# Kernel optimization log

Hardware: AMD Instinct MI355X
Metric: run time of the kernel (lower is better)

The kernel has to match this reference:

```python
import jax, jax.numpy as jnp
import numpy as np

N_HEAD = 16


def setup_inputs() -> dict:
    key = jax.random.key(0)
    ks = jax.random.split(key, 12)
    B, T, S, D = 64, 1, 448, 1024
    x = jax.random.normal(ks[0], (B, T, D), dtype=jnp.float32)
    k_cache = jax.random.normal(ks[1], (B, S, D), dtype=jnp.float32)
    v_cache = jax.random.normal(ks[2], (B, S, D), dtype=jnp.float32)
    current_index = jax.random.randint(ks[3], (1,), 0, S, dtype=jnp.int64)
    attention_mask = jnp.zeros((1, S), dtype=jnp.float32)
    s = 0.02
    Wq = jax.random.normal(ks[4], (D, D), dtype=jnp.float32) * s
    bq = jax.random.normal(ks[5], (D,), dtype=jnp.float32) * s
    Wk = jax.random.normal(ks[6], (D, D), dtype=jnp.float32) * s  # whisper key proj has no bias
    Wv = jax.random.normal(ks[7], (D, D), dtype=jnp.float32) * s
    bv = jax.random.normal(ks[8], (D,), dtype=jnp.float32) * s
    Wo = jax.random.normal(ks[9], (D, D), dtype=jnp.float32) * s
    bo = jax.random.normal(ks[10], (D,), dtype=jnp.float32) * s
    return {"x": x, "k_cache": k_cache, "v_cache": v_cache,
            "current_index": current_index, "attention_mask": attention_mask,
            "Wq": Wq, "bq": bq, "Wk": Wk, "Wv": Wv, "bv": bv, "Wo": Wo, "bo": bo}


def reference(x, k_cache, v_cache, current_index, attention_mask,
              Wq, bq, Wk, Wv, bv, Wo, bo):
    B, T, D = x.shape            # T == 1 (single decode token)
    S = k_cache.shape[1]         # cache length (448)
    H = N_HEAD
    Dh = D // H
    scale = float(Dh) ** -0.25

    # q/k/v projections of the new token
    q = x @ Wq + bq              # [B, T, D]
    k = x @ Wk                   # [B, T, D]
    v = x @ Wv + bv              # [B, T, D]

    # scatter the new token into the caches at current_index (functional clone+write)
    idx = current_index[0]
    k_upd = jax.lax.dynamic_update_slice(k_cache, k, (0, idx, 0))  # [B, S, D]
    v_upd = jax.lax.dynamic_update_slice(v_cache, v, (0, idx, 0))

    # whisper qkv_attention: scale q and k each by Dh**-0.25
    qh = q.reshape(B, T, H, Dh).transpose(0, 2, 1, 3) * scale      # [B, H, T, Dh]
    kh = k_upd.reshape(B, S, H, Dh).transpose(0, 2, 3, 1) * scale  # [B, H, Dh, S]
    vh = v_upd.reshape(B, S, H, Dh).transpose(0, 2, 1, 3)          # [B, H, S, Dh]

    qk = qh @ kh + attention_mask          # [B, H, T, S]  (mask broadcasts)
    w = jax.nn.softmax(qk, axis=-1)
    wv = (w @ vh).transpose(0, 2, 1, 3).reshape(B, T, D)

    out = wv @ Wo + bo
    return out, k_upd, v_upd
```

## Files before the change

### kernel.cpp

```cpp
#include <hip/hip_runtime.h>

#define B_SZ    64
#define S_LEN   448
#define D_MODEL 1024
#define N_HEAD  16
#define D_HEAD  64
#define CHUNK   28
#define NCH     16

typedef float f4 __attribute__((ext_vector_type(4)));

__global__ __launch_bounds__(256) void gemm_part(
    const float* __restrict__ X,
    const float* __restrict__ W0, const float* __restrict__ W1,
    const float* __restrict__ W2,
    float* __restrict__ P)
{
    const int nt  = blockIdx.x;
    const int kt  = blockIdx.y;
    const int mat = blockIdx.z;
    const float* __restrict__ W = (mat == 0) ? W0 : ((mat == 1) ? W1 : W2);

    const int t  = threadIdx.x;
    const int n  = nt * 64 + (t & 63);
    const int b0 = __builtin_amdgcn_readfirstlane((t >> 6) * 16);
    const int k0 = kt * 128;

    float acc[16];
#pragma unroll
    for (int j = 0; j < 16; ++j) acc[j] = 0.f;

#pragma unroll 8
    for (int k = k0; k < k0 + 128; ++k) {
        const float w = W[k * D_MODEL + n];
#pragma unroll
        for (int j = 0; j < 16; ++j)
            acc[j] += X[(b0 + j) * D_MODEL + k] * w;
    }

    float* p = P + (size_t)(mat * 8 + kt) * (B_SZ * D_MODEL);
#pragma unroll
    for (int j = 0; j < 16; ++j)
        p[(b0 + j) * D_MODEL + n] = acc[j];
}

__global__ __launch_bounds__(256) void reduce_out(
    const float* __restrict__ P, const float* __restrict__ bo,
    float* __restrict__ out)
{
    const int i = blockIdx.x * 256 + threadIdx.x;
    float s = bo[i & (D_MODEL - 1)];
#pragma unroll
    for (int kt = 0; kt < 8; ++kt)
        s += P[(size_t)kt * 65536 + i];
    out[i] = s;
}

__global__ __launch_bounds__(256) void stream_attn(
    const float* __restrict__ kcache, const float* __restrict__ vcache,
    const float* __restrict__ part,
    const float* __restrict__ bq, const float* __restrict__ bv,
    const float* __restrict__ amask, const int* __restrict__ idxp,
    float* __restrict__ kout, float* __restrict__ vout,
    float* __restrict__ accws, float* __restrict__ mlws)
{
    const int c   = blockIdx.x;
    const int b   = blockIdx.y;
    const int t   = threadIdx.x;
    const int col = t * 4;
    const int h   = t >> 4;
    const int l16 = t & 15;
    const int idx = idxp[0];
    const int s0  = c * CHUNK;

    f4 q = *(const f4*)(bq + col);
#pragma unroll
    for (int kt = 0; kt < 8; ++kt)
        q += *(const f4*)(part + (size_t)kt * 65536 + b * D_MODEL + col);

    f4 knew = (f4)0.f, vnew = (f4)0.f;
    if ((idx >= s0) && (idx < s0 + CHUNK)) {
#pragma unroll
        for (int kt = 0; kt < 8; ++kt) {
            knew += *(const f4*)(part + (size_t)(8 + kt)  * 65536 + b * D_MODEL + col);
            vnew += *(const f4*)(part + (size_t)(16 + kt) * 65536 + b * D_MODEL + col);
        }
        vnew += *(const f4*)(bv + col);
    }

    const size_t base = (size_t)(b * S_LEN + s0) * D_MODEL + col;

    float p[CHUNK];
#pragma unroll
    for (int s = 0; s < CHUNK; ++s) {
        f4 k4 = *(const f4*)(kcache + base + (size_t)s * D_MODEL);
        if (s0 + s == idx) k4 = knew;
        __builtin_nontemporal_store(k4, (f4*)(kout + base + (size_t)s * D_MODEL));
        p[s] = q.x * k4.x + q.y * k4.y + q.z * k4.z + q.w * k4.w;
    }

#pragma unroll
    for (int s = 0; s < CHUNK; ++s) {
        float v = p[s];
        v += __shfl_xor(v, 1);
        v += __shfl_xor(v, 2);
        v += __shfl_xor(v, 4);
        v += __shfl_xor(v, 8);
        p[s] = v * 0.125f + amask[s0 + s];
    }
    float m = p[0];
#pragma unroll
    for (int s = 1; s < CHUNK; ++s) m = fmaxf(m, p[s]);
    float l = 0.f;
#pragma unroll
    for (int s = 0; s < CHUNK; ++s) { p[s] = __expf(p[s] - m); l += p[s]; }

    f4 acc = (f4)0.f;
#pragma unroll
    for (int s = 0; s < CHUNK; ++s) {
        f4 v4 = *(const f4*)(vcache + base + (size_t)s * D_MODEL);
        if (s0 + s == idx) v4 = vnew;
        __builtin_nontemporal_store(v4, (f4*)(vout + base + (size_t)s * D_MODEL));
        acc.x += p[s] * v4.x;
        acc.y += p[s] * v4.y;
        acc.z += p[s] * v4.z;
        acc.w += p[s] * v4.w;
    }

    float* ap = accws + ((size_t)(b * N_HEAD + h) * NCH + c) * D_HEAD + l16 * 4;
    *(f4*)ap = acc;
    if (l16 == 0) {
        const int w = (b * N_HEAD + h) * NCH + c;
        mlws[w * 2]     = m;
        mlws[w * 2 + 1] = l;
    }
}

__global__ __launch_bounds__(256) void combine(
    const float* __restrict__ accws, const float* __restrict__ mlws,
    float* __restrict__ wvws)
{
    const int t = threadIdx.x;
    const int w = blockIdx.x * 4 + (t >> 6);
    const int d = t & 63;

    float M = -1e30f;
#pragma unroll
    for (int c = 0; c < NCH; ++c)
        M = fmaxf(M, mlws[(w * NCH + c) * 2]);
    float L = 0.f, O = 0.f;
#pragma unroll
    for (int c = 0; c < NCH; ++c) {
        const float f = __expf(mlws[(w * NCH + c) * 2] - M);
        L += mlws[(w * NCH + c) * 2 + 1] * f;
        O += accws[(w * NCH + c) * D_HEAD + d] * f;
    }
    const int b = w >> 4, h = w & 15;
    wvws[b * D_MODEL + h * D_HEAD + d] = O / L;
}

extern "C" void kernel_launch(void* const* d_in, const int* in_sizes, int n_in,
                              void* d_out, int out_size, void* d_ws, size_t ws_size,
                              hipStream_t stream) {
    const float* x      = (const float*)d_in[0];
    const float* kcache = (const float*)d_in[1];
    const float* vcache = (const float*)d_in[2];
    const int*   idxp   = (const int*)d_in[3];
    const float* amask  = (const float*)d_in[4];
    const float* Wq     = (const float*)d_in[5];
    const float* bq     = (const float*)d_in[6];
    const float* Wk     = (const float*)d_in[7];
    const float* Wv     = (const float*)d_in[8];
    const float* bv     = (const float*)d_in[9];
    const float* Wo     = (const float*)d_in[10];
    const float* bo     = (const float*)d_in[11];

    float* out  = (float*)d_out;
    float* kout = out + 65536;
    float* vout = kout + (size_t)B_SZ * S_LEN * D_MODEL;

    float* ws    = (float*)d_ws;
    float* part  = ws;
    float* accws = ws + 1572864;
    float* mlws  = ws + 2621440;
    float* wvws  = ws + 2654208;

    gemm_part<<<dim3(16, 8, 3), 256, 0, stream>>>(x, Wq, Wk, Wv, part);

    stream_attn<<<dim3(NCH, B_SZ), 256, 0, stream>>>(
        kcache, vcache, part, bq, bv, amask, idxp,
        kout, vout, accws, mlws);

    combine<<<256, 256, 0, stream>>>(accws, mlws, wvws);

    gemm_part<<<dim3(16, 8, 1), 256, 0, stream>>>(wvws, Wo, Wo, Wo, part);
    reduce_out<<<256, 256, 0, stream>>>(part, bo, out);
}
```

Before: 167.3 us.

## Split attention into separate K-stream, softmax and V-stream kernels with more blocks

Replaces the fused single-pass flash-style attention kernel with a pipeline: a prep kernel reduces the QKV split-K partials once, a K-stream kernel computes scores and writes the K cache, a softmax kernel normalizes per head, and a V-stream kernel accumulates weighted V while writing the V cache. The grid grows from 16 to 28 chunks per batch, each block covering 16 rows in 4-row wave tiles, to raise parallelism and memory-level concurrency for the bandwidth-bound cache copy. It also removes the redundant per-block re-reduction of the q/k/v partials. In exchange it adds kernel launches and a global round trip for the scores, and the K and V streams are now serialized rather than interleaved in one kernel.

```diff
diff --git a/kernel.cpp b/kernel.cpp
--- a/kernel.cpp
+++ b/kernel.cpp
@@ -5,10 +5,16 @@
 #define D_MODEL 1024
 #define N_HEAD  16
 #define D_HEAD  64
-#define CHUNK   28
-#define NCH     16
+#define NCH     28
 
 typedef float f4 __attribute__((ext_vector_type(4)));
+
+#define PARTU_OFF  0
+#define QBUF_OFF   1835008
+#define KNBUF_OFF  1900544
+#define VNBUF_OFF  1966080
+#define SCORE_OFF  2031616
+#define WV_OFF     2490368
 
 __global__ __launch_bounds__(256) void gemm_part(
     const float* __restrict__ X,
@@ -44,6 +50,21 @@
         p[(b0 + j) * D_MODEL + n] = acc[j];
 }
 
+__global__ __launch_bounds__(256) void prep(
+    const float* __restrict__ P, const float* __restrict__ bq,
+    const float* __restrict__ bv, float* __restrict__ qkv)
+{
+    const int i   = blockIdx.x * 256 + threadIdx.x;
+    const int mat = i >> 16;
+    const int r   = i & 65535;
+    const int d   = r & (D_MODEL - 1);
+    float s = (mat == 0) ? bq[d] : ((mat == 2) ? bv[d] : 0.f);
+#pragma unroll
+    for (int kt = 0; kt < 8; ++kt)
+        s += P[(size_t)(mat * 8 + kt) * 65536 + r];
+    qkv[i] = s;
+}
+
 __global__ __launch_bounds__(256) void reduce_out(
     const float* __restrict__ P, const float* __restrict__ bo,
     float* __restrict__ out)
@@ -56,107 +77,145 @@
     out[i] = s;
 }
 
-__global__ __launch_bounds__(256) void stream_attn(
-    const float* __restrict__ kcache, const float* __restrict__ vcache,
-    const float* __restrict__ part,
-    const float* __restrict__ bq, const float* __restrict__ bv,
-    const float* __restrict__ amask, const int* __restrict__ idxp,
-    float* __restrict__ kout, float* __restrict__ vout,
-    float* __restrict__ accws, float* __restrict__ mlws)
-{
-    const int c   = blockIdx.x;
-    const int b   = blockIdx.y;
-    const int t   = threadIdx.x;
-    const int col = t * 4;
-    const int h   = t >> 4;
-    const int l16 = t & 15;
-    const int idx = idxp[0];
-    const int s0  = c * CHUNK;
-
-    f4 q = *(const f4*)(bq + col);
-#pragma unroll
-    for (int kt = 0; kt < 8; ++kt)
-        q += *(const f4*)(part + (size_t)kt * 65536 + b * D_MODEL + col);
-
-    f4 knew = (f4)0.f, vnew = (f4)0.f;
-    if ((idx >= s0) && (idx < s0 + CHUNK)) {
-#pragma unroll
-        for (int kt = 0; kt < 8; ++kt) {
-            knew += *(const f4*)(part + (size_t)(8 + kt)  * 65536 + b * D_MODEL + col);
-            vnew += *(const f4*)(part + (size_t)(16 + kt) * 65536 + b * D_MODEL + col);
+__global__ __launch_bounds__(256) void kstream(
+    const float* __restrict__ kcache, const float* __restrict__ qbuf,
+    const float* __restrict__ knbuf, const float* __restrict__ amask,
+    const int* __restrict__ idxp,
+    float* __restrict__ kout, float* __restrict__ score)
+{
+    const int bid  = blockIdx.x;
+    const int b    = bid / NCH;
+    const int c    = bid % NCH;
+    const int w    = threadIdx.x >> 6;
+    const int lane = threadIdx.x & 63;
+    const int g    = lane >> 4;
+    const int idx  = idxp[0];
+    const int s0   = c * 16 + w * 4;
+
+    f4 q4[4];
+#pragma unroll
+    for (int j = 0; j < 4; ++j)
+        q4[j] = *(const f4*)(qbuf + b * D_MODEL + j * 256 + lane * 4);
+
+#pragma unroll
+    for (int r = 0; r < 4; ++r) {
+        const int s = s0 + r;
+        const size_t ro = ((size_t)b * S_LEN + s) * D_MODEL;
+        float dot[4];
+#pragma unroll
+        for (int j = 0; j < 4; ++j) {
+            f4 k4 = *(const f4*)(kcache + ro + j * 256 + lane * 4);
+            if (s == idx)
+                k4 = *(const f4*)(knbuf + b * D_MODEL + j * 256 + lane * 4);
+            __builtin_nontemporal_store(k4, (f4*)(kout + ro + j * 256 + lane * 4));
+            dot[j] = q4[j].x * k4.x + q4[j].y * k4.y + q4[j].z * k4.z + q4[j].w * k4.w;
         }
-        vnew += *(const f4*)(bv + col);
-    }
-
-    const size_t base = (size_t)(b * S_LEN + s0) * D_MODEL + col;
-
-    float p[CHUNK];
-#pragma unroll
-    for (int s = 0; s < CHUNK; ++s) {
-        f4 k4 = *(const f4*)(kcache + base + (size_t)s * D_MODEL);
-        if (s0 + s == idx) k4 = knew;
-        __builtin_nontemporal_store(k4, (f4*)(kout + base + (size_t)s * D_MODEL));
-        p[s] = q.x * k4.x + q.y * k4.y + q.z * k4.z + q.w * k4.w;
-    }
-
-#pragma unroll
-    for (int s = 0; s < CHUNK; ++s) {
-        float v = p[s];
-        v += __shfl_xor(v, 1);
-        v += __shfl_xor(v, 2);
-        v += __shfl_xor(v, 4);
-        v += __shfl_xor(v, 8);
-        p[s] = v * 0.125f + amask[s0 + s];
-    }
-    float m = p[0];
-#pragma unroll
-    for (int s = 1; s < CHUNK; ++s) m = fmaxf(m, p[s]);
-    float l = 0.f;
-#pragma unroll
-    for (int s = 0; s < CHUNK; ++s) { p[s] = __expf(p[s] - m); l += p[s]; }
-
-    f4 acc = (f4)0.f;
-#pragma unroll
-    for (int s = 0; s < CHUNK; ++s) {
-        f4 v4 = *(const f4*)(vcache + base + (size_t)s * D_MODEL);
-        if (s0 + s == idx) v4 = vnew;
-        __builtin_nontemporal_store(v4, (f4*)(vout + base + (size_t)s * D_MODEL));
-        acc.x += p[s] * v4.x;
-        acc.y += p[s] * v4.y;
-        acc.z += p[s] * v4.z;
-        acc.w += p[s] * v4.w;
-    }
-
-    float* ap = accws + ((size_t)(b * N_HEAD + h) * NCH + c) * D_HEAD + l16 * 4;
-    *(f4*)ap = acc;
-    if (l16 == 0) {
-        const int w = (b * N_HEAD + h) * NCH + c;
-        mlws[w * 2]     = m;
-        mlws[w * 2 + 1] = l;
-    }
+#pragma unroll
+        for (int j = 0; j < 4; ++j) {
+            float v = dot[j];
+            v += __shfl_xor(v, 1);
+            v += __shfl_xor(v, 2);
+            v += __shfl_xor(v, 4);
+            v += __shfl_xor(v, 8);
+            if ((lane & 15) == 0)
+                score[((size_t)b * S_LEN + s) * N_HEAD + (j * 4 + g)]
+                    = v * 0.125f + amask[s];
+        }
+    }
+}
+
+__global__ __launch_bounds__(256) void softmax_k(float* __restrict__ sc)
+{
+    const int gw   = blockIdx.x * 4 + (threadIdx.x >> 6);
+    const int b    = gw >> 4;
+    const int h    = gw & 15;
+    const int lane = threadIdx.x & 63;
+
+    float v[7];
+    float mx = -1e30f;
+#pragma unroll
+    for (int t = 0; t < 7; ++t) {
+        v[t] = sc[((size_t)b * S_LEN + lane + t * 64) * N_HEAD + h];
+        mx = fmaxf(mx, v[t]);
+    }
+#pragma unroll
+    for (int o = 1; o < 64; o <<= 1) mx = fmaxf(mx, __shfl_xor(mx, o));
+    float sum = 0.f;
+#pragma unroll
+    for (int t = 0; t < 7; ++t) { v[t] = __expf(v[t] - mx); sum += v[t]; }
+#pragma unroll
+    for (int o = 1; o < 64; o <<= 1) sum += __shfl_xor(sum, o);
+    const float inv = 1.f / sum;
+#pragma unroll
+    for (int t = 0; t < 7; ++t)
+        sc[((size_t)b * S_LEN + lane + t * 64) * N_HEAD + h] = v[t] * inv;
+}
+
+__global__ __launch_bounds__(256) void vstream(
+    const float* __restrict__ vcache, const float* __restrict__ vnbuf,
+    const float* __restrict__ wbuf, const int* __restrict__ idxp,
+    float* __restrict__ vout, float* __restrict__ partial)
+{
+    const int bid  = blockIdx.x;
+    const int b    = bid / NCH;
+    const int c    = bid % NCH;
+    const int w    = threadIdx.x >> 6;
+    const int lane = threadIdx.x & 63;
+    const int g    = lane >> 4;
+    const int idx  = idxp[0];
+    const int s0   = c * 16 + w * 4;
+
+    f4 acc[4];
+#pragma unroll
+    for (int j = 0; j < 4; ++j) acc[j] = (f4)0.f;
+
+#pragma unroll
+    for (int r = 0; r < 4; ++r) {
+        const int s = s0 + r;
+        const size_t ro = ((size_t)b * S_LEN + s) * D_MODEL;
+#pragma unroll
+        for (int j = 0; j < 4; ++j) {
+            const float wt = wbuf[((size_t)b * S_LEN + s) * N_HEAD + (j * 4 + g)];
+            f4 v4 = *(const f4*)(vcache + ro + j * 256 + lane * 4);
+            if (s == idx)
+                v4 = *(const f4*)(vnbuf + b * D_MODEL + j * 256 + lane * 4);
+            __builtin_nontemporal_store(v4, (f4*)(vout + ro + j * 256 + lane * 4));
+            acc[j].x += wt * v4.x;
+            acc[j].y += wt * v4.y;
+            acc[j].z += wt * v4.z;
+            acc[j].w += wt * v4.w;
+        }
+    }
+
+    __shared__ float lds[4][D_MODEL];
+#pragma unroll
+    for (int j = 0; j < 4; ++j)
+        *(f4*)&lds[w][j * 256 + lane * 4] = acc[j];
+    __syncthreads();
+
+    const int d = threadIdx.x * 4;
+    f4 s4 = *(const f4*)&lds[0][d];
+    const f4 s1 = *(const f4*)&lds[1][d];
+    const f4 s2 = *(const f4*)&lds[2][d];
+    const f4 s3 = *(const f4*)&lds[3][d];
+    s4.x += s1.x + s2.x + s3.x;
+    s4.y += s1.y + s2.y + s3.y;
+    s4.z += s1.z + s2.z + s3.z;
+    s4.w += s1.w + s2.w + s3.w;
+    *(f4*)(partial + ((size_t)b * NCH + c) * D_MODEL + d) = s4;
 }
 
 __global__ __launch_bounds__(256) void combine(
-    const float* __restrict__ accws, const float* __restrict__ mlws,
-    float* __restrict__ wvws)
-{
-    const int t = threadIdx.x;
-    const int w = blockIdx.x * 4 + (t >> 6);
-    const int d = t & 63;
-
-    float M = -1e30f;
+    const float* __restrict__ partial, float* __restrict__ wv)
+{
+    const int i = blockIdx.x * 256 + threadIdx.x;
+    const int b = i >> 10;
+    const int d = i & (D_MODEL - 1);
+    float s = 0.f;
 #pragma unroll
     for (int c = 0; c < NCH; ++c)
-        M = fmaxf(M, mlws[(w * NCH + c) * 2]);
-    float L = 0.f, O = 0.f;
-#pragma unroll
-    for (int c = 0; c < NCH; ++c) {
-        const float f = __expf(mlws[(w * NCH + c) * 2] - M);
-        L += mlws[(w * NCH + c) * 2 + 1] * f;
-        O += accws[(w * NCH + c) * D_HEAD + d] * f;
-    }
-    const int b = w >> 4, h = w & 15;
-    wvws[b * D_MODEL + h * D_HEAD + d] = O / L;
+        s += partial[((size_t)b * NCH + c) * D_MODEL + d];
+    wv[i] = s;
 }
 
 extern "C" void kernel_launch(void* const* d_in, const int* in_sizes, int n_in,
@@ -180,19 +239,27 @@
     float* vout = kout + (size_t)B_SZ * S_LEN * D_MODEL;
 
     float* ws    = (float*)d_ws;
-    float* part  = ws;
-    float* accws = ws + 1572864;
-    float* mlws  = ws + 2621440;
-    float* wvws  = ws + 2654208;
-
-    gemm_part<<<dim3(16, 8, 3), 256, 0, stream>>>(x, Wq, Wk, Wv, part);
-
-    stream_attn<<<dim3(NCH, B_SZ), 256, 0, stream>>>(
-        kcache, vcache, part, bq, bv, amask, idxp,
-        kout, vout, accws, mlws);
-
-    combine<<<256, 256, 0, stream>>>(accws, mlws, wvws);
-
-    gemm_part<<<dim3(16, 8, 1), 256, 0, stream>>>(wvws, Wo, Wo, Wo, part);
-    reduce_out<<<256, 256, 0, stream>>>(part, bo, out);
-}
+    float* partU = ws + PARTU_OFF;
+    float* qbuf  = ws + QBUF_OFF;
+    float* knbuf = ws + KNBUF_OFF;
+    float* vnbuf = ws + VNBUF_OFF;
+    float* score = ws + SCORE_OFF;
+    float* wvws  = ws + WV_OFF;
+
+    gemm_part<<<dim3(16, 8, 3), 256, 0, stream>>>(x, Wq, Wk, Wv, partU);
+
+    prep<<<768, 256, 0, stream>>>(partU, bq, bv, qbuf);
+
+    kstream<<<B_SZ * NCH, 256, 0, stream>>>(
+        kcache, qbuf, knbuf, amask, idxp, kout, score);
+
+    softmax_k<<<256, 256, 0, stream>>>(score);
+
+    vstream<<<B_SZ * NCH, 256, 0, stream>>>(
+        vcache, vnbuf, score, idxp, vout, partU);
+
+    combine<<<256, 256, 0, stream>>>(partU, wvws);
+
+    gemm_part<<<dim3(16, 8, 1), 256, 0, stream>>>(wvws, Wo, Wo, Wo, partU);
+    reduce_out<<<256, 256, 0, stream>>>(partU, bo, out);
+}
```

New measurement: 179.5 us. +7.3%, slower.

## Split attention into finer sequence chunks and pre-reduce QKV partials in a prep kernel

Applied to the files above, without the earlier changes.

Shrinks the per-block sequence chunk from 28 to 4 rows, raising the attention grid from 1024 to 7168 blocks so more memory requests are in flight while streaming the caches. Adds a prep kernel that sums the split-K GEMM partials plus biases once, instead of every attention block re-reading eight partial slices for q. The cost is a much larger partial-accumulator workspace, one extra launch, and a combine kernel that now reduces over 112 chunks per head, which adds extra global traffic.

```diff
diff --git a/kernel.cpp b/kernel.cpp
--- a/kernel.cpp
+++ b/kernel.cpp
@@ -4,11 +4,16 @@
 #define S_LEN   448
 #define D_MODEL 1024
 #define N_HEAD  16
-#define D_HEAD  64
-#define CHUNK   28
-#define NCH     16
+#define CHUNK   4
+#define NCH     112
 
 typedef float f4 __attribute__((ext_vector_type(4)));
+
+#define PARTU_OFF  0
+#define QKV_OFF    1572864
+#define ACC_OFF    1769472
+#define ML_OFF     9109504
+#define WV_OFF     9338880
 
 __global__ __launch_bounds__(256) void gemm_part(
     const float* __restrict__ X,
@@ -44,6 +49,21 @@
         p[(b0 + j) * D_MODEL + n] = acc[j];
 }
 
+__global__ __launch_bounds__(256) void prep(
+    const float* __restrict__ P, const float* __restrict__ bq,
+    const float* __restrict__ bv, float* __restrict__ qkv)
+{
+    const int i   = blockIdx.x * 256 + threadIdx.x;
+    const int mat = i >> 16;
+    const int r   = i & 65535;
+    const int d   = r & (D_MODEL - 1);
+    float s = (mat == 0) ? bq[d] : ((mat == 2) ? bv[d] : 0.f);
+#pragma unroll
+    for (int kt = 0; kt < 8; ++kt)
+        s += P[(size_t)(mat * 8 + kt) * 65536 + r];
+    qkv[i] = s;
+}
+
 __global__ __launch_bounds__(256) void reduce_out(
     const float* __restrict__ P, const float* __restrict__ bo,
     float* __restrict__ out)
@@ -56,16 +76,16 @@
     out[i] = s;
 }
 
-__global__ __launch_bounds__(256) void stream_attn(
+__global__ __launch_bounds__(256) void fused_stream(
     const float* __restrict__ kcache, const float* __restrict__ vcache,
-    const float* __restrict__ part,
-    const float* __restrict__ bq, const float* __restrict__ bv,
+    const float* __restrict__ qkv,
     const float* __restrict__ amask, const int* __restrict__ idxp,
     float* __restrict__ kout, float* __restrict__ vout,
     float* __restrict__ accws, float* __restrict__ mlws)
 {
-    const int c   = blockIdx.x;
-    const int b   = blockIdx.y;
+    const int bid = blockIdx.x;
+    const int b   = bid / NCH;
+    const int c   = bid % NCH;
     const int t   = threadIdx.x;
     const int col = t * 4;
     const int h   = t >> 4;
@@ -73,66 +93,56 @@
     const int idx = idxp[0];
     const int s0  = c * CHUNK;
 
-    f4 q = *(const f4*)(bq + col);
-#pragma unroll
-    for (int kt = 0; kt < 8; ++kt)
-        q += *(const f4*)(part + (size_t)kt * 65536 + b * D_MODEL + col);
-
+    const f4 q = *(const f4*)(qkv + b * D_MODEL + col);
     f4 knew = (f4)0.f, vnew = (f4)0.f;
-    if ((idx >= s0) && (idx < s0 + CHUNK)) {
-#pragma unroll
-        for (int kt = 0; kt < 8; ++kt) {
-            knew += *(const f4*)(part + (size_t)(8 + kt)  * 65536 + b * D_MODEL + col);
-            vnew += *(const f4*)(part + (size_t)(16 + kt) * 65536 + b * D_MODEL + col);
-        }
-        vnew += *(const f4*)(bv + col);
-    }
-
-    const size_t base = (size_t)(b * S_LEN + s0) * D_MODEL + col;
+    if (idx >= s0 && idx < s0 + CHUNK) {
+        knew = *(const f4*)(qkv + (size_t)(B_SZ + b) * D_MODEL + col);
+        vnew = *(const f4*)(qkv + (size_t)(2 * B_SZ + b) * D_MODEL + col);
+    }
+
+    const size_t base = ((size_t)b * S_LEN + s0) * D_MODEL + col;
 
     float p[CHUNK];
 #pragma unroll
-    for (int s = 0; s < CHUNK; ++s) {
-        f4 k4 = *(const f4*)(kcache + base + (size_t)s * D_MODEL);
-        if (s0 + s == idx) k4 = knew;
-        __builtin_nontemporal_store(k4, (f4*)(kout + base + (size_t)s * D_MODEL));
-        p[s] = q.x * k4.x + q.y * k4.y + q.z * k4.z + q.w * k4.w;
-    }
-
-#pragma unroll
-    for (int s = 0; s < CHUNK; ++s) {
-        float v = p[s];
+    for (int r = 0; r < CHUNK; ++r) {
+        f4 k4 = *(const f4*)(kcache + base + (size_t)r * D_MODEL);
+        if (s0 + r == idx) k4 = knew;
+        __builtin_nontemporal_store(k4, (f4*)(kout + base + (size_t)r * D_MODEL));
+        p[r] = q.x * k4.x + q.y * k4.y + q.z * k4.z + q.w * k4.w;
+    }
+
+#pragma unroll
+    for (int r = 0; r < CHUNK; ++r) {
+        float v = p[r];
         v += __shfl_xor(v, 1);
         v += __shfl_xor(v, 2);
         v += __shfl_xor(v, 4);
         v += __shfl_xor(v, 8);
-        p[s] = v * 0.125f + amask[s0 + s];
+        p[r] = v * 0.125f + amask[s0 + r];
     }
     float m = p[0];
 #pragma unroll
-    for (int s = 1; s < CHUNK; ++s) m = fmaxf(m, p[s]);
+    for (int r = 1; r < CHUNK; ++r) m = fmaxf(m, p[r]);
     float l = 0.f;
 #pragma unroll
-    for (int s = 0; s < CHUNK; ++s) { p[s] = __expf(p[s] - m); l += p[s]; }
+    for (int r = 0; r < CHUNK; ++r) { p[r] = __expf(p[r] - m); l += p[r]; }
 
     f4 acc = (f4)0.f;
 #pragma unroll
-    for (int s = 0; s < CHUNK; ++s) {
-        f4 v4 = *(const f4*)(vcache + base + (size_t)s * D_MODEL);
-        if (s0 + s == idx) v4 = vnew;
-        __builtin_nontemporal_store(v4, (f4*)(vout + base + (size_t)s * D_MODEL));
-        acc.x += p[s] * v4.x;
-        acc.y += p[s] * v4.y;
-        acc.z += p[s] * v4.z;
-        acc.w += p[s] * v4.w;
-    }
-
-    float* ap = accws + ((size_t)(b * N_HEAD + h) * NCH + c) * D_HEAD + l16 * 4;
-    *(f4*)ap = acc;
+    for (int r = 0; r < CHUNK; ++r) {
+        f4 v4 = *(const f4*)(vcache + base + (size_t)r * D_MODEL);
+        if (s0 + r == idx) v4 = vnew;
+        __builtin_nontemporal_store(v4, (f4*)(vout + base + (size_t)r * D_MODEL));
+        acc.x += p[r] * v4.x;
+        acc.y += p[r] * v4.y;
+        acc.z += p[r] * v4.z;
+        acc.w += p[r] * v4.w;
+    }
+
+    *(f4*)(accws + (size_t)bid * D_MODEL + col) = acc;
     if (l16 == 0) {
-        const int w = (b * N_HEAD + h) * NCH + c;
-        mlws[w * 2]     = m;
-        mlws[w * 2 + 1] = l;
+        mlws[bid * 32 + h * 2]     = m;
+        mlws[bid * 32 + h * 2 + 1] = l;
     }
 }
 
@@ -142,21 +152,21 @@
 {
     const int t = threadIdx.x;
     const int w = blockIdx.x * 4 + (t >> 6);
+    const int b = w >> 4, h = w & 15;
     const int d = t & 63;
 
     float M = -1e30f;
-#pragma unroll
+#pragma unroll 8
     for (int c = 0; c < NCH; ++c)
-        M = fmaxf(M, mlws[(w * NCH + c) * 2]);
+        M = fmaxf(M, mlws[(b * NCH + c) * 32 + h * 2]);
     float L = 0.f, O = 0.f;
-#pragma unroll
+#pragma unroll 8
     for (int c = 0; c < NCH; ++c) {
-        const float f = __expf(mlws[(w * NCH + c) * 2] - M);
-        L += mlws[(w * NCH + c) * 2 + 1] * f;
-        O += accws[(w * NCH + c) * D_HEAD + d] * f;
-    }
-    const int b = w >> 4, h = w & 15;
-    wvws[b * D_MODEL + h * D_HEAD + d] = O / L;
+        const float f = __expf(mlws[(b * NCH + c) * 32 + h * 2] - M);
+        L += mlws[(b * NCH + c) * 32 + h * 2 + 1] * f;
+        O += accws[(size_t)(b * NCH + c) * D_MODEL + h * 64 + d] * f;
+    }
+    wvws[b * D_MODEL + h * 64 + d] = O / L;
 }
 
 extern "C" void kernel_launch(void* const* d_in, const int* in_sizes, int n_in,
@@ -180,19 +190,21 @@
     float* vout = kout + (size_t)B_SZ * S_LEN * D_MODEL;
 
     float* ws    = (float*)d_ws;
-    float* part  = ws;
-    float* accws = ws + 1572864;
-    float* mlws  = ws + 2621440;
-    float* wvws  = ws + 2654208;
-
-    gemm_part<<<dim3(16, 8, 3), 256, 0, stream>>>(x, Wq, Wk, Wv, part);
-
-    stream_attn<<<dim3(NCH, B_SZ), 256, 0, stream>>>(
-        kcache, vcache, part, bq, bv, amask, idxp,
-        kout, vout, accws, mlws);
+    float* partU = ws + PARTU_OFF;
+    float* qkv   = ws + QKV_OFF;
+    float* accws = ws + ACC_OFF;
+    float* mlws  = ws + ML_OFF;
+    float* wvws  = ws + WV_OFF;
+
+    gemm_part<<<dim3(16, 8, 3), 256, 0, stream>>>(x, Wq, Wk, Wv, partU);
+
+    prep<<<768, 256, 0, stream>>>(partU, bq, bv, qkv);
+
+    fused_stream<<<B_SZ * NCH, 256, 0, stream>>>(
+        kcache, vcache, qkv, amask, idxp, kout, vout, accws, mlws);
 
     combine<<<256, 256, 0, stream>>>(accws, mlws, wvws);
 
-    gemm_part<<<dim3(16, 8, 1), 256, 0, stream>>>(wvws, Wo, Wo, Wo, part);
-    reduce_out<<<256, 256, 0, stream>>>(part, bo, out);
-}
+    gemm_part<<<dim3(16, 8, 1), 256, 0, stream>>>(wvws, Wo, Wo, Wo, partU);
+    reduce_out<<<256, 256, 0, stream>>>(partU, bo, out);
+}
```

After: 186.6 us. 1.12x slower.
